# Performance work log

Measured on AMD Instinct MI355X. Metric: run time of the kernel, lower is better.

## Reference

```python
import jax, jax.numpy as jnp
import numpy as np

DIM = 768
HEADS = 12
HEAD_DIM = DIM // HEADS
HIDDEN = 4 * DIM
EPS = 1e-5


def layernorm(x, g, b):
    mu = jnp.mean(x, axis=-1, keepdims=True)
    var = jnp.var(x, axis=-1, keepdims=True)
    return (x - mu) * jax.lax.rsqrt(var + EPS) * g + b


def setup_inputs() -> dict:
    key = jax.random.key(0)
    ks = jax.random.split(key, 16)
    s = 0.02
    return {
        "x_pre": jax.random.normal(ks[0], (8, 512, DIM), jnp.float32),
        "x_post": jax.random.normal(ks[1], (8, 512, DIM), jnp.float32),
        "attention_mask": jnp.zeros((8, 1, 1024, 1024), jnp.float32),
        "ln1_g": jnp.ones((DIM,), jnp.float32),
        "ln1_b": jnp.zeros((DIM,), jnp.float32),
        "Wq": jax.random.normal(ks[2], (DIM, DIM), jnp.float32) * s,
        "bq": jnp.zeros((DIM,), jnp.float32),
        "Wk": jax.random.normal(ks[3], (DIM, DIM), jnp.float32) * s,
        "bk": jnp.zeros((DIM,), jnp.float32),
        "Wv": jax.random.normal(ks[4], (DIM, DIM), jnp.float32) * s,
        "bv": jnp.zeros((DIM,), jnp.float32),
        "Wo": jax.random.normal(ks[5], (DIM, DIM), jnp.float32) * s,
        "bo": jnp.zeros((DIM,), jnp.float32),
        "ln2_g": jnp.ones((DIM,), jnp.float32),
        "ln2_b": jnp.zeros((DIM,), jnp.float32),
        "W1": jax.random.normal(ks[6], (DIM, HIDDEN), jnp.float32) * s,
        "b1": jnp.zeros((HIDDEN,), jnp.float32),
        "W2": jax.random.normal(ks[7], (HIDDEN, DIM), jnp.float32) * s,
        "b2": jnp.zeros((DIM,), jnp.float32),
        "gamma_1": 0.1 * jnp.ones((DIM,), jnp.float32),
        "gamma_2": 0.1 * jnp.ones((DIM,), jnp.float32),
    }


def reference(x_pre, x_post, attention_mask, ln1_g, ln1_b, Wq, bq, Wk, bk, Wv, bv,
              Wo, bo, ln2_g, ln2_b, W1, b1, W2, b2, gamma_1, gamma_2):
    x = jnp.concatenate((x_pre, x_post), axis=1)  # [B, N, C]
    B, N, C = x.shape
    h = layernorm(x, ln1_g, ln1_b)
    # self-attention with manual QK^T in float32
    q = (h @ Wq + bq).reshape(B, N, HEADS, HEAD_DIM)
    k = (h @ Wk + bk).reshape(B, N, HEADS, HEAD_DIM)
    v = (h @ Wv + bv).reshape(B, N, HEADS, HEAD_DIM)
    scale = HEAD_DIM ** -0.5
    attn = jnp.einsum("bqhd,bkhd->bhqk", q.astype(jnp.float32) * scale,
                      k.astype(jnp.float32)) + attention_mask
    attn = jax.nn.softmax(attn, axis=-1).astype(x.dtype)
    o = jnp.einsum("bhqk,bkhd->bqhd", attn, v).reshape(B, N, C)
    o = o @ Wo + bo
    x = x + gamma_1 * o
    # MLP
    h2 = layernorm(x, ln2_g, ln2_b)
    h2 = jax.nn.gelu(h2 @ W1 + b1, approximate=False) @ W2 + b2
    return x + gamma_2 * h2
```

## Files before the change

### kernel.cpp

```cpp
#include <hip/hip_runtime.h>
#include <hip/hip_fp8.h>
#include <cstdint>
#include <cstddef>

#define BATCH   8
#define SEQ     1024
#define DIMC    768
#define HEADS   12
#define HDIM    64
#define HIDDEN  3072
#define MROWS   (BATCH * SEQ)
#define L2E     1.4426950408889634f

typedef __attribute__((ext_vector_type(8))) short bf16x8;
typedef __attribute__((ext_vector_type(4))) float f32x4;

__device__ __forceinline__ unsigned short f2b(float f) {
    union { float f; unsigned int u; } v; v.f = f;
    unsigned int u = v.u;
    return (unsigned short)((u + 0x7FFFu + ((u >> 16) & 1u)) >> 16);
}
__device__ __forceinline__ unsigned char f2e4m3(float f) {
    __hip_fp8_e4m3 t(f); return t.__x;
}
__device__ __forceinline__ unsigned int b2u(float f) {
    union { float f; unsigned int u; } v; v.f = f; return v.u;
}
__device__ __forceinline__ float u2f(unsigned int u) {
    union { unsigned int u; float f; } v; v.u = u; return v.f;
}
__device__ __forceinline__ void gl_lds16(const void* g, void* l) {
    __builtin_amdgcn_global_load_lds(
        (const __attribute__((address_space(1))) unsigned int*)g,
        (__attribute__((address_space(3))) unsigned int*)l, 16, 0, 0);
}
__device__ __forceinline__ float gelu_fast(float x) {
    float p = x * x;
    float a = fmaf(p, 0.044715f, 1.0f);
    float w = x * a * -2.302118131f;
    float z = exp2f(w);
    return x * __builtin_amdgcn_rcpf(1.0f + z);
}

__global__ __launch_bounds__(256) void tcvt_k(const float* __restrict__ src,
                                              unsigned char* __restrict__ dst,
                                              int K, int N) {
    __shared__ float tile[32][33];
    int k0 = blockIdx.y * 32, n0 = blockIdx.x * 32;
    int tx = threadIdx.x, ty = threadIdx.y;
#pragma unroll
    for (int i = 0; i < 4; i++)
        tile[ty + i * 8][tx] = src[(size_t)(k0 + ty + i * 8) * N + n0 + tx];
    __syncthreads();
#pragma unroll
    for (int i = 0; i < 4; i++)
        dst[(size_t)(n0 + ty + i * 8) * K + k0 + tx] = f2e4m3(tile[tx][ty + i * 8]);
}

__global__ __launch_bounds__(256) void tcvt4_k(const float* __restrict__ s0,
                                               const float* __restrict__ s1,
                                               const float* __restrict__ s2,
                                               const float* __restrict__ s3,
                                               unsigned char* __restrict__ d0,
                                               unsigned char* __restrict__ d1,
                                               unsigned char* __restrict__ d2,
                                               unsigned char* __restrict__ d3) {
    const float* src = (blockIdx.z == 0) ? s0 : (blockIdx.z == 1) ? s1
                     : (blockIdx.z == 2) ? s2 : s3;
    unsigned char* dst = (blockIdx.z == 0) ? d0 : (blockIdx.z == 1) ? d1
                       : (blockIdx.z == 2) ? d2 : d3;
    __shared__ float tile[32][33];
    int k0 = blockIdx.y * 32, n0 = blockIdx.x * 32;
    int tx = threadIdx.x, ty = threadIdx.y;
#pragma unroll
    for (int i = 0; i < 4; i++)
        tile[ty + i * 8][tx] = src[(size_t)(k0 + ty + i * 8) * DIMC + n0 + tx];
    __syncthreads();
#pragma unroll
    for (int i = 0; i < 4; i++)
        dst[(size_t)(n0 + ty + i * 8) * DIMC + k0 + tx] = f2e4m3(tile[tx][ty + i * 8]);
}

__global__ __launch_bounds__(256) void vtr_k(const unsigned short* __restrict__ src,
                                             unsigned char* __restrict__ dst) {
    int bh = blockIdx.x, k0 = blockIdx.y * 64;
    __shared__ unsigned short t[64][68];
    const unsigned short* s = src + ((size_t)bh * SEQ + k0) * HDIM;
    unsigned char* d = dst + (size_t)bh * HDIM * SEQ + k0;
    int tid = threadIdx.x;
#pragma unroll
    for (int p = 0; p < 4; p++) {
        int c = p * 256 + tid;
        int key = c >> 4, dd = (c & 15) * 4;
        *(uint2*)&t[key][dd] = *(const uint2*)&s[key * HDIM + dd];
    }
    __syncthreads();
#pragma unroll
    for (int p = 0; p < 8; p++) {
        int idx = p * 256 + tid;
        int dd = idx >> 5, kk = (idx & 31) * 2;
        uchar2 o;
        o.x = f2e4m3(u2f((unsigned int)t[kk][dd] << 16));
        o.y = f2e4m3(u2f((unsigned int)t[kk + 1][dd] << 16));
        *(uchar2*)&d[(size_t)dd * SEQ + kk] = o;
    }
}

__global__ __launch_bounds__(256) void ln_k(const float* __restrict__ xa,
                                            const float* __restrict__ xb,
                                            const float* __restrict__ g,
                                            const float* __restrict__ bt,
                                            float* __restrict__ x_out,
                                            unsigned char* __restrict__ h_out) {
    int r = blockIdx.x;
    const float* src;
    if (xb) {
        int b = r >> 10, nn = r & 1023;
        src = (nn < 512) ? xa + ((size_t)b * 512 + nn) * DIMC
                         : xb + ((size_t)b * 512 + (nn - 512)) * DIMC;
    } else {
        src = xa + (size_t)r * DIMC;
    }
    int t = threadIdx.x;
    float v[3], s = 0.f, s2 = 0.f;
#pragma unroll
    for (int j = 0; j < 3; j++) {
        v[j] = src[t + j * 256];
        s += v[j]; s2 += v[j] * v[j];
    }
#pragma unroll
    for (int off = 32; off > 0; off >>= 1) {
        s  += __shfl_down(s,  off);
        s2 += __shfl_down(s2, off);
    }
    __shared__ float red[8];
    int wid = t >> 6, lane = t & 63;
    if (lane == 0) { red[wid] = s; red[4 + wid] = s2; }
    __syncthreads();
    s  = red[0] + red[1] + red[2] + red[3];
    s2 = red[4] + red[5] + red[6] + red[7];
    float mu  = s * (1.f / DIMC);
    float var = s2 * (1.f / DIMC) - mu * mu;
    float rstd = rsqrtf(var + 1e-5f);
#pragma unroll
    for (int j = 0; j < 3; j++) {
        int i = t + j * 256;
        float xv = v[j];
        if (x_out) x_out[(size_t)r * DIMC + i] = xv;
        h_out[(size_t)r * DIMC + i] = f2e4m3((xv - mu) * rstd * g[i] + bt[i]);
    }
}

template <int MODE, int TM>
__global__ __launch_bounds__(256) void gemm_k(
    const unsigned char* __restrict__ A,
    const unsigned char* __restrict__ Bt0,
    const unsigned char* __restrict__ Bt1,
    const unsigned char* __restrict__ Bt2,
    const float* __restrict__ bias0,
    const float* __restrict__ bias1,
    const float* __restrict__ bias2,
    const float* __restrict__ resid,
    const float* __restrict__ gamma,
    float* __restrict__ outf,
    unsigned short* __restrict__ outb0,
    unsigned short* __restrict__ outb1,
    unsigned short* __restrict__ outb2,
    unsigned char* __restrict__ outc,
    int K, int ldo) {

    constexpr int AI = TM / 32;
    const int tid  = threadIdx.x;
    const int wid  = tid >> 6, lane = tid & 63;
    const int quad = lane >> 4, l16 = lane & 15;
    const int m0 = blockIdx.y * TM, n0 = blockIdx.x * 128;
    const int waveM = (wid >> 1) * (AI * 16), waveN = (wid & 1) * 64;

    const unsigned char* Bt = Bt0;
    if (MODE == 0) Bt = (blockIdx.z == 0) ? Bt0 : (blockIdx.z == 1) ? Bt1 : Bt2;

    __shared__ __align__(16) unsigned char As[TM * 128];
    __shared__ __align__(16) unsigned char Bs[128 * 128];

    int carow[AI], caoff[AI], cbrow[4], cboff[4];
#pragma unroll
    for (int j = 0; j < AI; j++) {
        int c = j * 256 + tid;
        carow[j] = c >> 3;
        caoff[j] = ((c & 7) ^ (carow[j] & 7)) * 16;
    }
#pragma unroll
    for (int j = 0; j < 4; j++) {
        int c = j * 256 + tid;
        cbrow[j] = c >> 3;
        cboff[j] = ((c & 7) ^ (cbrow[j] & 7)) * 16;
    }
    const int asw = l16 & 7;
    int abase[AI], bbase[4];
#pragma unroll
    for (int i = 0; i < AI; i++)
        abase[i] = (waveM + i * 16 + l16) * 128 + (quad & 1) * 8;
#pragma unroll
    for (int i = 0; i < 4; i++)
        bbase[i] = (waveN + i * 16 + l16) * 128 + (quad & 1) * 8;

    f32x4 acc[AI][4] = {};

    for (int k0 = 0; k0 < K; k0 += 128) {
#pragma unroll
        for (int j = 0; j < AI; j++)
            gl_lds16(&A[(size_t)(m0 + carow[j]) * K + k0 + caoff[j]],
                     &As[(j * 256 + wid * 64) * 16]);
#pragma unroll
        for (int j = 0; j < 4; j++)
            gl_lds16(&Bt[(size_t)(n0 + cbrow[j]) * K + k0 + cboff[j]],
                     &Bs[(j * 256 + wid * 64) * 16]);
        __syncthreads();

#pragma unroll
        for (int kk = 0; kk < 4; kk++) {
            const int csw = ((kk * 2 + (quad >> 1)) ^ asw) * 16;
            long a[AI], b[4];
#pragma unroll
            for (int i = 0; i < AI; i++) a[i] = *(const long*)&As[abase[i] + csw];
#pragma unroll
            for (int i = 0; i < 4; i++) b[i] = *(const long*)&Bs[bbase[i] + csw];
#pragma unroll
            for (int i = 0; i < AI; i++)
#pragma unroll
                for (int j = 0; j < 4; j++)
                    acc[i][j] = __builtin_amdgcn_mfma_f32_16x16x32_fp8_fp8(
                        a[i], b[j], acc[i][j], 0, 0, 0);
        }
        __syncthreads();
    }

    const float* bias = bias0;
    unsigned short* outb = outb0;
    if (MODE == 0) {
        bias = (blockIdx.z == 0) ? bias0 : (blockIdx.z == 1) ? bias1 : bias2;
        outb = (blockIdx.z == 0) ? outb0 : (blockIdx.z == 1) ? outb1 : outb2;
    }
    const float qscale = 0.125f * L2E;
#pragma unroll
    for (int i = 0; i < AI; i++) {
#pragma unroll
        for (int j = 0; j < 4; j++) {
            int n = n0 + waveN + j * 16 + l16;
#pragma unroll
            for (int r = 0; r < 4; r++) {
                int m = m0 + waveM + i * 16 + quad * 4 + r;
                float val = acc[i][j][r];
                if (MODE == 0) {
                    val += bias[n];
                    if (blockIdx.z == 0) val *= qscale;
                    int bb = m >> 10, nn = m & 1023;
                    int hh = n >> 6,  d  = n & 63;
                    outb[(((size_t)bb * HEADS + hh) * SEQ + nn) * HDIM + d] = f2b(val);
                } else if (MODE == 1 || MODE == 3) {
                    val += bias[n];
                    outf[(size_t)m * ldo + n] =
                        resid[(size_t)m * ldo + n] + gamma[n] * val;
                } else {
                    outc[(size_t)m * ldo + n] = f2e4m3(gelu_fast(val + bias[n]));
                }
            }
        }
    }
}

__global__ __launch_bounds__(256) void attn_k(const unsigned short* __restrict__ Q,
                                              const unsigned short* __restrict__ Km,
                                              const unsigned char* __restrict__ Vt,
                                              const float* __restrict__ mask,
                                              unsigned char* __restrict__ O) {
    const int bh = blockIdx.x;
    const int b = bh / HEADS, h = bh - b * HEADS;
    const int tid = threadIdx.x;
    const int wid = tid >> 6, lane = tid & 63;
    const int quad = lane >> 4, l16 = lane & 15;
    const int qw = blockIdx.y * 64 + wid * 16;

    __shared__ __align__(16) unsigned short Ks[128 * 64];
    __shared__ __align__(16) unsigned char  Vs[64 * 128];
    __shared__ __align__(16) unsigned char  Ps[4][16 * 136];
    unsigned char* sp = Ps[wid];

    const unsigned short* Qp = Q + ((size_t)bh * SEQ + qw) * HDIM;
    bf16x8 aQ[2];
    aQ[0] = *(const bf16x8*)(Qp + l16 * HDIM + quad * 8);
    aQ[1] = *(const bf16x8*)(Qp + l16 * HDIM + 32 + quad * 8);

    int kql[4], vql[2];
#pragma unroll
    for (int j = 0; j < 4; j++) {
        int ck = (wid * 4 + j) * 64 + lane;
        int key = ck >> 3, ch = ck & 7;
        kql[j] = key * HDIM + ((ch ^ ((key >> 3) & 7)) * 8);
    }
#pragma unroll
    for (int j = 0; j < 2; j++) {
        int cv = j * 256 + wid * 64 + lane;
        int d = cv >> 3, ch = cv & 7;
        vql[j] = d * SEQ + ((ch ^ (d & 7)) * 16);
    }
    const unsigned short* Kb = Km + (size_t)bh * SEQ * HDIM;
    const unsigned char*  Vb = Vt + (size_t)bh * HDIM * SEQ;
    const float* Mbase = mask + (size_t)b * SEQ * SEQ
                       + (size_t)(qw + quad * 4) * SEQ + 8 * l16;

    f32x4 o[4] = {};
    f32x4 osum = {};
    const long ONES = 0x3838383838383838L;

    for (int key0 = 0; key0 < SEQ; key0 += 128) {
        float mreg[4][8];
        const float* mb = Mbase + key0;
#pragma unroll
        for (int r = 0; r < 4; r++) {
            float4 u0 = *(const float4*)(mb + r * SEQ);
            float4 u1 = *(const float4*)(mb + r * SEQ + 4);
            mreg[r][0] = u0.x; mreg[r][1] = u0.y; mreg[r][2] = u0.z; mreg[r][3] = u0.w;
            mreg[r][4] = u1.x; mreg[r][5] = u1.y; mreg[r][6] = u1.z; mreg[r][7] = u1.w;
        }
        const unsigned short* Kg = Kb + (size_t)key0 * HDIM;
        const unsigned char*  Vg = Vb + key0;
#pragma unroll
        for (int j = 0; j < 4; j++)
            gl_lds16(Kg + kql[j], &Ks[(wid * 4 + j) * 512]);
#pragma unroll
        for (int j = 0; j < 2; j++)
            gl_lds16(Vg + vql[j], &Vs[(j * 256 + wid * 64) * 16]);
        __syncthreads();

        f32x4 s[8];
#pragma unroll
        for (int nt = 0; nt < 8; nt++) {
            const unsigned short* kp = &Ks[(8 * l16 + nt) * 64];
            bf16x8 b0 = *(const bf16x8*)&kp[(quad ^ (l16 & 7)) * 8];
            bf16x8 b1 = *(const bf16x8*)&kp[((4 + quad) ^ (l16 & 7)) * 8];
            f32x4 t = {};
            t = __builtin_amdgcn_mfma_f32_16x16x32_bf16(aQ[0], b0, t, 0, 0, 0);
            t = __builtin_amdgcn_mfma_f32_16x16x32_bf16(aQ[1], b1, t, 0, 0, 0);
            s[nt] = t;
        }

#pragma unroll
        for (int r = 0; r < 4; r++) {
            float e[8];
#pragma unroll
            for (int nt = 0; nt < 8; nt++)
                e[nt] = exp2f(fmaf(mreg[r][nt], L2E, s[nt][r]));
            unsigned int d0 = __builtin_amdgcn_cvt_pk_fp8_f32(e[0], e[1], 0, false);
            d0 = __builtin_amdgcn_cvt_pk_fp8_f32(e[2], e[3], d0, true);
            unsigned int d1 = __builtin_amdgcn_cvt_pk_fp8_f32(e[4], e[5], 0, false);
            d1 = __builtin_amdgcn_cvt_pk_fp8_f32(e[6], e[7], d1, true);
            int prow = quad * 4 + r;
            uint2 pv; pv.x = d0; pv.y = d1;
            *(uint2*)&sp[prow * 136 + ((l16 ^ (prow & 7)) * 8)] = pv;
        }
        __builtin_amdgcn_wave_barrier();

        long aP[4];
#pragma unroll
        for (int kt = 0; kt < 4; kt++)
            aP[kt] = *(const long*)&sp[l16 * 136 + (((kt * 4 + quad) ^ (l16 & 7)) * 8)];
#pragma unroll
        for (int kt = 0; kt < 4; kt++)
            osum = __builtin_amdgcn_mfma_f32_16x16x32_fp8_fp8(aP[kt], ONES, osum, 0, 0, 0);
#pragma unroll
        for (int dt = 0; dt < 4; dt++) {
            const unsigned char* vp = &Vs[(dt * 16 + l16) * 128];
            f32x4 oo = o[dt];
#pragma unroll
            for (int kt = 0; kt < 4; kt++) {
                long bv = *(const long*)
                    &vp[(((kt * 2 + (quad >> 1)) ^ (l16 & 7)) * 16) + (quad & 1) * 8];
                oo = __builtin_amdgcn_mfma_f32_16x16x32_fp8_fp8(aP[kt], bv, oo, 0, 0, 0);
            }
            o[dt] = oo;
        }
        __syncthreads();
    }

#pragma unroll
    for (int r = 0; r < 4; r++) {
        float inv = 1.0f / osum[r];
#pragma unroll
        for (int dt = 0; dt < 4; dt++)
            O[(size_t)(b * SEQ + qw + quad * 4 + r) * DIMC + h * HDIM + dt * 16 + l16] =
                f2e4m3(o[dt][r] * inv);
    }
}

extern "C" void kernel_launch(void* const* d_in, const int* in_sizes, int n_in,
                              void* d_out, int out_size, void* d_ws, size_t ws_size,
                              hipStream_t stream) {
    const float* x_pre = (const float*)d_in[0];
    const float* x_post= (const float*)d_in[1];
    const float* mask  = (const float*)d_in[2];
    const float* ln1g  = (const float*)d_in[3];
    const float* ln1b  = (const float*)d_in[4];
    const float* Wq    = (const float*)d_in[5];
    const float* bq    = (const float*)d_in[6];
    const float* Wk    = (const float*)d_in[7];
    const float* bk    = (const float*)d_in[8];
    const float* Wv    = (const float*)d_in[9];
    const float* bv    = (const float*)d_in[10];
    const float* Wo    = (const float*)d_in[11];
    const float* bo    = (const float*)d_in[12];
    const float* ln2g  = (const float*)d_in[13];
    const float* ln2b  = (const float*)d_in[14];
    const float* W1    = (const float*)d_in[15];
    const float* b1    = (const float*)d_in[16];
    const float* W2    = (const float*)d_in[17];
    const float* b2    = (const float*)d_in[18];
    const float* g1    = (const float*)d_in[19];
    const float* g2    = (const float*)d_in[20];
    float* out = (float*)d_out;

    char* p = (char*)d_ws;
    float* xf  = (float*)p;                  p += (size_t)MROWS * DIMC * 4;
    float* x2f = (float*)p;                  p += (size_t)MROWS * DIMC * 4;
    unsigned char* h8  = (unsigned char*)p;  p += (size_t)MROWS * DIMC;
    unsigned char* O8  = (unsigned char*)p;  p += (size_t)MROWS * DIMC;
    unsigned char* G8  = (unsigned char*)p;  p += (size_t)MROWS * HIDDEN;
    unsigned short* Qb = (unsigned short*)p; p += (size_t)MROWS * DIMC * 2;
    unsigned short* Kb = (unsigned short*)p; p += (size_t)MROWS * DIMC * 2;
    unsigned short* Vb = (unsigned short*)p; p += (size_t)MROWS * DIMC * 2;
    unsigned char* V8  = (unsigned char*)p;  p += (size_t)MROWS * DIMC;
    unsigned char* Wq8 = (unsigned char*)p;  p += (size_t)DIMC * DIMC;
    unsigned char* Wk8 = (unsigned char*)p;  p += (size_t)DIMC * DIMC;
    unsigned char* Wv8 = (unsigned char*)p;  p += (size_t)DIMC * DIMC;
    unsigned char* Wo8 = (unsigned char*)p;  p += (size_t)DIMC * DIMC;
    unsigned char* W18 = (unsigned char*)p;  p += (size_t)DIMC * HIDDEN;
    unsigned char* W28 = (unsigned char*)p;  p += (size_t)DIMC * HIDDEN;

    dim3 tb(32, 8);
    tcvt4_k<<<dim3(24, 24, 4), tb, 0, stream>>>(Wq, Wk, Wv, Wo, Wq8, Wk8, Wv8, Wo8);
    tcvt_k<<<dim3(96, 24), tb, 0, stream>>>(W1, W18, DIMC, HIDDEN);
    tcvt_k<<<dim3(24, 96), tb, 0, stream>>>(W2, W28, HIDDEN, DIMC);

    ln_k<<<MROWS, 256, 0, stream>>>(x_pre, x_post, ln1g, ln1b, xf, h8);

    gemm_k<0, 128><<<dim3(6, 64, 3), 256, 0, stream>>>(h8, Wq8, Wk8, Wv8,
        bq, bk, bv, nullptr, nullptr, nullptr, Qb, Kb, Vb, nullptr, DIMC, DIMC);

    vtr_k<<<dim3(96, 16), 256, 0, stream>>>(Vb, V8);

    attn_k<<<dim3(96, 16), 256, 0, stream>>>(Qb, Kb, V8, mask, O8);

    gemm_k<1, 64><<<dim3(6, 128), 256, 0, stream>>>(O8, Wo8, nullptr, nullptr,
        bo, nullptr, nullptr, xf, g1, x2f, nullptr, nullptr, nullptr, nullptr, DIMC, DIMC);

    ln_k<<<MROWS, 256, 0, stream>>>(x2f, nullptr, ln2g, ln2b, nullptr, h8);

    gemm_k<2, 128><<<dim3(24, 64), 256, 0, stream>>>(h8, W18, nullptr, nullptr,
        b1, nullptr, nullptr, nullptr, nullptr, nullptr, nullptr, nullptr, nullptr,
        G8, DIMC, HIDDEN);

    gemm_k<3, 64><<<dim3(6, 128), 256, 0, stream>>>(G8, W28, nullptr, nullptr,
        b2, nullptr, nullptr, x2f, g2, out, nullptr, nullptr, nullptr, nullptr,
        HIDDEN, DIMC);

    (void)in_sizes; (void)n_in; (void)out_size; (void)ws_size;
}
```

Before: 381.4 us.

## Double-buffer K/V tiles in attention and remap blocks so each XCD serves one batch

The attention kernel now ping-pongs two LDS buffers for K and V and prefetches the next mask tile into registers while the current tile is computed, so global-to-LDS loads overlap the MFMA and exp work. Block indices are also remapped so that blocks landing on the same XCD (flat index mod 8) all handle one batch, aiming for better L2 reuse of that batch's mask and K/V. In exchange, LDS use doubles and register pressure grows from holding two mask tiles, which may lower occupancy. The remap assumes a grid of 96 by 16 blocks.

```diff
diff --git a/kernel.cpp b/kernel.cpp
--- a/kernel.cpp
+++ b/kernel.cpp
@@ -269,20 +269,80 @@
     }
 }
 
+__device__ __forceinline__ void attn_tile(
+    const unsigned short* __restrict__ KsB,
+    const unsigned char*  __restrict__ VsB,
+    unsigned char* __restrict__ sp,
+    bf16x8 aQ0, bf16x8 aQ1,
+    const float (&M)[4][8],
+    int quad, int l16,
+    f32x4 (&o)[4], f32x4& osum)
+{
+    const long ONES = 0x3838383838383838L;
+    f32x4 s[8];
+#pragma unroll
+    for (int nt = 0; nt < 8; nt++) {
+        const unsigned short* kp = &KsB[(8 * l16 + nt) * 64];
+        bf16x8 b0 = *(const bf16x8*)&kp[(quad ^ (l16 & 7)) * 8];
+        bf16x8 b1 = *(const bf16x8*)&kp[((4 + quad) ^ (l16 & 7)) * 8];
+        f32x4 t = {};
+        t = __builtin_amdgcn_mfma_f32_16x16x32_bf16(aQ0, b0, t, 0, 0, 0);
+        t = __builtin_amdgcn_mfma_f32_16x16x32_bf16(aQ1, b1, t, 0, 0, 0);
+        s[nt] = t;
+    }
+#pragma unroll
+    for (int r = 0; r < 4; r++) {
+        float e[8];
+#pragma unroll
+        for (int nt = 0; nt < 8; nt++)
+            e[nt] = exp2f(fmaf(M[r][nt], L2E, s[nt][r]));
+        unsigned int d0 = __builtin_amdgcn_cvt_pk_fp8_f32(e[0], e[1], 0, false);
+        d0 = __builtin_amdgcn_cvt_pk_fp8_f32(e[2], e[3], d0, true);
+        unsigned int d1 = __builtin_amdgcn_cvt_pk_fp8_f32(e[4], e[5], 0, false);
+        d1 = __builtin_amdgcn_cvt_pk_fp8_f32(e[6], e[7], d1, true);
+        int prow = quad * 4 + r;
+        uint2 pv; pv.x = d0; pv.y = d1;
+        *(uint2*)&sp[prow * 136 + ((l16 ^ (prow & 7)) * 8)] = pv;
+    }
+    __builtin_amdgcn_wave_barrier();
+    long aP[4];
+#pragma unroll
+    for (int kt = 0; kt < 4; kt++)
+        aP[kt] = *(const long*)&sp[l16 * 136 + (((kt * 4 + quad) ^ (l16 & 7)) * 8)];
+#pragma unroll
+    for (int kt = 0; kt < 4; kt++)
+        osum = __builtin_amdgcn_mfma_f32_16x16x32_fp8_fp8(aP[kt], ONES, osum, 0, 0, 0);
+#pragma unroll
+    for (int dt = 0; dt < 4; dt++) {
+        const unsigned char* vp = &VsB[(dt * 16 + l16) * 128];
+        f32x4 oo = o[dt];
+#pragma unroll
+        for (int kt = 0; kt < 4; kt++) {
+            long bv = *(const long*)
+                &vp[(((kt * 2 + (quad >> 1)) ^ (l16 & 7)) * 16) + (quad & 1) * 8];
+            oo = __builtin_amdgcn_mfma_f32_16x16x32_fp8_fp8(aP[kt], bv, oo, 0, 0, 0);
+        }
+        o[dt] = oo;
+    }
+}
+
 __global__ __launch_bounds__(256) void attn_k(const unsigned short* __restrict__ Q,
                                               const unsigned short* __restrict__ Km,
                                               const unsigned char* __restrict__ Vt,
                                               const float* __restrict__ mask,
                                               unsigned char* __restrict__ O) {
-    const int bh = blockIdx.x;
-    const int b = bh / HEADS, h = bh - b * HEADS;
+    const int flat = blockIdx.y * 96 + blockIdx.x;
+    const int xcd  = flat & 7, slot = flat >> 3;
+    const int h = slot % 12, y = slot / 12;
+    const int b = xcd;
+    const int bh = b * HEADS + h;
     const int tid = threadIdx.x;
     const int wid = tid >> 6, lane = tid & 63;
     const int quad = lane >> 4, l16 = lane & 15;
-    const int qw = blockIdx.y * 64 + wid * 16;
-
-    __shared__ __align__(16) unsigned short Ks[128 * 64];
-    __shared__ __align__(16) unsigned char  Vs[64 * 128];
+    const int qw = y * 64 + wid * 16;
+
+    __shared__ __align__(16) unsigned short Ks[2][128 * 64];
+    __shared__ __align__(16) unsigned char  Vs[2][64 * 128];
     __shared__ __align__(16) unsigned char  Ps[4][16 * 136];
     unsigned char* sp = Ps[wid];
 
@@ -309,79 +369,52 @@
     const float* Mbase = mask + (size_t)b * SEQ * SEQ
                        + (size_t)(qw + quad * 4) * SEQ + 8 * l16;
 
+#define ATTN_STAGE(BUF, K0) do {                                              \
+        const unsigned short* Kg_ = Kb + (size_t)(K0) * HDIM;                 \
+        const unsigned char*  Vg_ = Vb + (K0);                                \
+        _Pragma("unroll")                                                     \
+        for (int j = 0; j < 4; j++)                                           \
+            gl_lds16(Kg_ + kql[j], &Ks[BUF][(wid * 4 + j) * 512]);            \
+        _Pragma("unroll")                                                     \
+        for (int j = 0; j < 2; j++)                                           \
+            gl_lds16(Vg_ + vql[j], &Vs[BUF][(j * 256 + wid * 64) * 16]);      \
+    } while (0)
+
+#define ATTN_MASK(M, K0) do {                                                 \
+        const float* mb_ = Mbase + (K0);                                      \
+        _Pragma("unroll")                                                     \
+        for (int r = 0; r < 4; r++) {                                         \
+            float4 u0 = *(const float4*)(mb_ + r * SEQ);                      \
+            float4 u1 = *(const float4*)(mb_ + r * SEQ + 4);                  \
+            M[r][0] = u0.x; M[r][1] = u0.y; M[r][2] = u0.z; M[r][3] = u0.w;   \
+            M[r][4] = u1.x; M[r][5] = u1.y; M[r][6] = u1.z; M[r][7] = u1.w;   \
+        }                                                                     \
+    } while (0)
+
     f32x4 o[4] = {};
     f32x4 osum = {};
-    const long ONES = 0x3838383838383838L;
-
-    for (int key0 = 0; key0 < SEQ; key0 += 128) {
-        float mreg[4][8];
-        const float* mb = Mbase + key0;
-#pragma unroll
-        for (int r = 0; r < 4; r++) {
-            float4 u0 = *(const float4*)(mb + r * SEQ);
-            float4 u1 = *(const float4*)(mb + r * SEQ + 4);
-            mreg[r][0] = u0.x; mreg[r][1] = u0.y; mreg[r][2] = u0.z; mreg[r][3] = u0.w;
-            mreg[r][4] = u1.x; mreg[r][5] = u1.y; mreg[r][6] = u1.z; mreg[r][7] = u1.w;
+    float mA[4][8], mB[4][8];
+
+    ATTN_STAGE(0, 0);
+    ATTN_MASK(mA, 0);
+    __syncthreads();
+
+#pragma unroll
+    for (int t2 = 0; t2 < SEQ / 256; t2++) {
+        const int te = t2 * 256;
+        ATTN_STAGE(1, te + 128);
+        ATTN_MASK(mB, te + 128);
+        attn_tile(Ks[0], Vs[0], sp, aQ[0], aQ[1], mA, quad, l16, o, osum);
+        __syncthreads();
+        if (t2 + 1 < SEQ / 256) {
+            ATTN_STAGE(0, te + 256);
+            ATTN_MASK(mA, te + 256);
         }
-        const unsigned short* Kg = Kb + (size_t)key0 * HDIM;
-        const unsigned char*  Vg = Vb + key0;
-#pragma unroll
-        for (int j = 0; j < 4; j++)
-            gl_lds16(Kg + kql[j], &Ks[(wid * 4 + j) * 512]);
-#pragma unroll
-        for (int j = 0; j < 2; j++)
-            gl_lds16(Vg + vql[j], &Vs[(j * 256 + wid * 64) * 16]);
+        attn_tile(Ks[1], Vs[1], sp, aQ[0], aQ[1], mB, quad, l16, o, osum);
         __syncthreads();
-
-        f32x4 s[8];
-#pragma unroll
-        for (int nt = 0; nt < 8; nt++) {
-            const unsigned short* kp = &Ks[(8 * l16 + nt) * 64];
-            bf16x8 b0 = *(const bf16x8*)&kp[(quad ^ (l16 & 7)) * 8];
-            bf16x8 b1 = *(const bf16x8*)&kp[((4 + quad) ^ (l16 & 7)) * 8];
-            f32x4 t = {};
-            t = __builtin_amdgcn_mfma_f32_16x16x32_bf16(aQ[0], b0, t, 0, 0, 0);
-            t = __builtin_amdgcn_mfma_f32_16x16x32_bf16(aQ[1], b1, t, 0, 0, 0);
-            s[nt] = t;
-        }
-
-#pragma unroll
-        for (int r = 0; r < 4; r++) {
-            float e[8];
-#pragma unroll
-            for (int nt = 0; nt < 8; nt++)
-                e[nt] = exp2f(fmaf(mreg[r][nt], L2E, s[nt][r]));
-            unsigned int d0 = __builtin_amdgcn_cvt_pk_fp8_f32(e[0], e[1], 0, false);
-            d0 = __builtin_amdgcn_cvt_pk_fp8_f32(e[2], e[3], d0, true);
-            unsigned int d1 = __builtin_amdgcn_cvt_pk_fp8_f32(e[4], e[5], 0, false);
-            d1 = __builtin_amdgcn_cvt_pk_fp8_f32(e[6], e[7], d1, true);
-            int prow = quad * 4 + r;
-            uint2 pv; pv.x = d0; pv.y = d1;
-            *(uint2*)&sp[prow * 136 + ((l16 ^ (prow & 7)) * 8)] = pv;
-        }
-        __builtin_amdgcn_wave_barrier();
-
-        long aP[4];
-#pragma unroll
-        for (int kt = 0; kt < 4; kt++)
-            aP[kt] = *(const long*)&sp[l16 * 136 + (((kt * 4 + quad) ^ (l16 & 7)) * 8)];
-#pragma unroll
-        for (int kt = 0; kt < 4; kt++)
-            osum = __builtin_amdgcn_mfma_f32_16x16x32_fp8_fp8(aP[kt], ONES, osum, 0, 0, 0);
-#pragma unroll
-        for (int dt = 0; dt < 4; dt++) {
-            const unsigned char* vp = &Vs[(dt * 16 + l16) * 128];
-            f32x4 oo = o[dt];
-#pragma unroll
-            for (int kt = 0; kt < 4; kt++) {
-                long bv = *(const long*)
-                    &vp[(((kt * 2 + (quad >> 1)) ^ (l16 & 7)) * 16) + (quad & 1) * 8];
-                oo = __builtin_amdgcn_mfma_f32_16x16x32_fp8_fp8(aP[kt], bv, oo, 0, 0, 0);
-            }
-            o[dt] = oo;
-        }
-        __syncthreads();
-    }
+    }
+#undef ATTN_STAGE
+#undef ATTN_MASK
 
 #pragma unroll
     for (int r = 0; r < 4; r++) {
```

New measurement: 381.4 us. About the same (-0.0%).

## Prefetch next K/V tile into registers and remap attention blocks per XCD

Applied to the files above, without the earlier changes.

The attention kernel now software-pipelines K/V loading. The next tile is loaded into registers during compute on the current one and written to LDS after a barrier, replacing direct global-to-LDS copies followed by a sync. It also splits the score computation into two halves so exp/convert work interleaves with the MFMAs, and remaps the flat block index so each batch maps to one XCD for L2 locality. Launch bounds request 4 blocks per CU, which raises register pressure risk alongside the extra prefetch registers.

```diff
diff --git a/kernel.cpp b/kernel.cpp
--- a/kernel.cpp
+++ b/kernel.cpp
@@ -269,17 +269,20 @@
     }
 }
 
-__global__ __launch_bounds__(256) void attn_k(const unsigned short* __restrict__ Q,
-                                              const unsigned short* __restrict__ Km,
-                                              const unsigned char* __restrict__ Vt,
-                                              const float* __restrict__ mask,
-                                              unsigned char* __restrict__ O) {
-    const int bh = blockIdx.x;
-    const int b = bh / HEADS, h = bh - b * HEADS;
+__global__ __launch_bounds__(256, 4) void attn_k(const unsigned short* __restrict__ Q,
+                                                 const unsigned short* __restrict__ Km,
+                                                 const unsigned char* __restrict__ Vt,
+                                                 const float* __restrict__ mask,
+                                                 unsigned char* __restrict__ O) {
+    const int flat = blockIdx.y * 96 + blockIdx.x;
+    const int xcd  = flat & 7, slot = flat >> 3;
+    const int h = slot % 12, y = slot / 12;
+    const int b = xcd;
+    const int bh = b * HEADS + h;
     const int tid = threadIdx.x;
     const int wid = tid >> 6, lane = tid & 63;
     const int quad = lane >> 4, l16 = lane & 15;
-    const int qw = blockIdx.y * 64 + wid * 16;
+    const int qw = y * 64 + wid * 16;
 
     __shared__ __align__(16) unsigned short Ks[128 * 64];
     __shared__ __align__(16) unsigned char  Vs[64 * 128];
@@ -291,72 +294,107 @@
     aQ[0] = *(const bf16x8*)(Qp + l16 * HDIM + quad * 8);
     aQ[1] = *(const bf16x8*)(Qp + l16 * HDIM + 32 + quad * 8);
 
-    int kql[4], vql[2];
+    int kqb[4], vqb[2];
 #pragma unroll
     for (int j = 0; j < 4; j++) {
         int ck = (wid * 4 + j) * 64 + lane;
         int key = ck >> 3, ch = ck & 7;
-        kql[j] = key * HDIM + ((ch ^ ((key >> 3) & 7)) * 8);
+        kqb[j] = key * 128 + ((ch ^ ((key >> 3) & 7)) * 16);
     }
 #pragma unroll
     for (int j = 0; j < 2; j++) {
         int cv = j * 256 + wid * 64 + lane;
         int d = cv >> 3, ch = cv & 7;
-        vql[j] = d * SEQ + ((ch ^ (d & 7)) * 16);
-    }
-    const unsigned short* Kb = Km + (size_t)bh * SEQ * HDIM;
-    const unsigned char*  Vb = Vt + (size_t)bh * HDIM * SEQ;
+        vqb[j] = d * SEQ + ((ch ^ (d & 7)) * 16);
+    }
+    const char* Kb = (const char*)(Km + (size_t)bh * SEQ * HDIM);
+    const char* Vb = (const char*)(Vt + (size_t)bh * HDIM * SEQ);
     const float* Mbase = mask + (size_t)b * SEQ * SEQ
                        + (size_t)(qw + quad * 4) * SEQ + 8 * l16;
+
+    uint4 kst[4], vst[2];
+#define ATTN_LOADR(K0) do {                                                   \
+        const char* Kg_ = Kb + (size_t)(K0) * 128;                            \
+        const char* Vg_ = Vb + (K0);                                          \
+        _Pragma("unroll")                                                     \
+        for (int j = 0; j < 4; j++)                                           \
+            kst[j] = *(const uint4*)(Kg_ + kqb[j]);                           \
+        _Pragma("unroll")                                                     \
+        for (int j = 0; j < 2; j++)                                           \
+            vst[j] = *(const uint4*)(Vg_ + vqb[j]);                           \
+    } while (0)
+
+#define ATTN_WRITER() do {                                                    \
+        _Pragma("unroll")                                                     \
+        for (int j = 0; j < 4; j++)                                           \
+            *(uint4*)((char*)Ks + (wid * 4 + j) * 1024 + lane * 16) = kst[j]; \
+        _Pragma("unroll")                                                     \
+        for (int j = 0; j < 2; j++)                                           \
+            *(uint4*)((char*)Vs + (j * 256 + wid * 64 + lane) * 16) = vst[j]; \
+    } while (0)
 
     f32x4 o[4] = {};
     f32x4 osum = {};
     const long ONES = 0x3838383838383838L;
 
-    for (int key0 = 0; key0 < SEQ; key0 += 128) {
-        float mreg[4][8];
-        const float* mb = Mbase + key0;
+    ATTN_LOADR(0);
+    ATTN_WRITER();
+    __syncthreads();
+
+#pragma unroll
+    for (int t = 0; t < SEQ / 128; t++) {
+        if (t < SEQ / 128 - 1) ATTN_LOADR((t + 1) * 128);
+
+        const float* mb_ = Mbase + t * 128;
+        float4 mu0[4], mu1[4];
 #pragma unroll
         for (int r = 0; r < 4; r++) {
-            float4 u0 = *(const float4*)(mb + r * SEQ);
-            float4 u1 = *(const float4*)(mb + r * SEQ + 4);
-            mreg[r][0] = u0.x; mreg[r][1] = u0.y; mreg[r][2] = u0.z; mreg[r][3] = u0.w;
-            mreg[r][4] = u1.x; mreg[r][5] = u1.y; mreg[r][6] = u1.z; mreg[r][7] = u1.w;
-        }
-        const unsigned short* Kg = Kb + (size_t)key0 * HDIM;
-        const unsigned char*  Vg = Vb + key0;
-#pragma unroll
-        for (int j = 0; j < 4; j++)
-            gl_lds16(Kg + kql[j], &Ks[(wid * 4 + j) * 512]);
-#pragma unroll
-        for (int j = 0; j < 2; j++)
-            gl_lds16(Vg + vql[j], &Vs[(j * 256 + wid * 64) * 16]);
-        __syncthreads();
-
-        f32x4 s[8];
-#pragma unroll
-        for (int nt = 0; nt < 8; nt++) {
+            mu0[r] = *(const float4*)(mb_ + r * SEQ);
+            mu1[r] = *(const float4*)(mb_ + r * SEQ + 4);
+        }
+
+        f32x4 sA[4];
+#pragma unroll
+        for (int nt = 0; nt < 4; nt++) {
             const unsigned short* kp = &Ks[(8 * l16 + nt) * 64];
             bf16x8 b0 = *(const bf16x8*)&kp[(quad ^ (l16 & 7)) * 8];
             bf16x8 b1 = *(const bf16x8*)&kp[((4 + quad) ^ (l16 & 7)) * 8];
-            f32x4 t = {};
-            t = __builtin_amdgcn_mfma_f32_16x16x32_bf16(aQ[0], b0, t, 0, 0, 0);
-            t = __builtin_amdgcn_mfma_f32_16x16x32_bf16(aQ[1], b1, t, 0, 0, 0);
-            s[nt] = t;
-        }
-
+            f32x4 tt = {};
+            tt = __builtin_amdgcn_mfma_f32_16x16x32_bf16(aQ[0], b0, tt, 0, 0, 0);
+            tt = __builtin_amdgcn_mfma_f32_16x16x32_bf16(aQ[1], b1, tt, 0, 0, 0);
+            sA[nt] = tt;
+        }
+        unsigned int dlo[4];
 #pragma unroll
         for (int r = 0; r < 4; r++) {
-            float e[8];
-#pragma unroll
-            for (int nt = 0; nt < 8; nt++)
-                e[nt] = exp2f(fmaf(mreg[r][nt], L2E, s[nt][r]));
-            unsigned int d0 = __builtin_amdgcn_cvt_pk_fp8_f32(e[0], e[1], 0, false);
-            d0 = __builtin_amdgcn_cvt_pk_fp8_f32(e[2], e[3], d0, true);
-            unsigned int d1 = __builtin_amdgcn_cvt_pk_fp8_f32(e[4], e[5], 0, false);
-            d1 = __builtin_amdgcn_cvt_pk_fp8_f32(e[6], e[7], d1, true);
+            float e0 = exp2f(fmaf(mu0[r].x, L2E, sA[0][r]));
+            float e1 = exp2f(fmaf(mu0[r].y, L2E, sA[1][r]));
+            float e2 = exp2f(fmaf(mu0[r].z, L2E, sA[2][r]));
+            float e3 = exp2f(fmaf(mu0[r].w, L2E, sA[3][r]));
+            unsigned int d0 = __builtin_amdgcn_cvt_pk_fp8_f32(e0, e1, 0, false);
+            dlo[r] = __builtin_amdgcn_cvt_pk_fp8_f32(e2, e3, d0, true);
+        }
+        f32x4 sB[4];
+#pragma unroll
+        for (int nt = 0; nt < 4; nt++) {
+            const unsigned short* kp = &Ks[(8 * l16 + 4 + nt) * 64];
+            bf16x8 b0 = *(const bf16x8*)&kp[(quad ^ (l16 & 7)) * 8];
+            bf16x8 b1 = *(const bf16x8*)&kp[((4 + quad) ^ (l16 & 7)) * 8];
+            f32x4 tt = {};
+            tt = __builtin_amdgcn_mfma_f32_16x16x32_bf16(aQ[0], b0, tt, 0, 0, 0);
+            tt = __builtin_amdgcn_mfma_f32_16x16x32_bf16(aQ[1], b1, tt, 0, 0, 0);
+            sB[nt] = tt;
+        }
+#pragma unroll
+        for (int r = 0; r < 4; r++) {
+            float e4 = exp2f(fmaf(mu1[r].x, L2E, sB[0][r]));
+            float e5 = exp2f(fmaf(mu1[r].y, L2E, sB[1][r]));
+            float e6 = exp2f(fmaf(mu1[r].z, L2E, sB[2][r]));
+            float e7 = exp2f(fmaf(mu1[r].w, L2E, sB[3][r]));
+            unsigned int d1 = __builtin_amdgcn_cvt_pk_fp8_f32(e4, e5, 0, false);
+            d1 = __builtin_amdgcn_cvt_pk_fp8_f32(e6, e7, d1, true);
             int prow = quad * 4 + r;
-            uint2 pv; pv.x = d0; pv.y = d1;
+            uint2 pv; pv.x = dlo[r]; pv.y = d1;
             *(uint2*)&sp[prow * 136 + ((l16 ^ (prow & 7)) * 8)] = pv;
         }
         __builtin_amdgcn_wave_barrier();
@@ -380,8 +418,15 @@
             }
             o[dt] = oo;
         }
+
         __syncthreads();
-    }
+        if (t < SEQ / 128 - 1) {
+            ATTN_WRITER();
+            __syncthreads();
+        }
+    }
+#undef ATTN_LOADR
+#undef ATTN_WRITER
 
 #pragma unroll
     for (int r = 0; r < 4; r++) {
```

After: 449.6 us. 17.9% more time.

## Double-buffer attention K/V tiles in LDS and remap blocks across XCDs

Applied to the files above, without the earlier changes.

The attention kernel now processes 64-key tiles with two LDS buffers, prefetching the next K/V tile while computing the current one, instead of a single 128-key buffer loaded and synchronised each iteration. Block indices are also remapped so blocks of the same batch land on the same XCD, aiming at better L2 reuse of K/V and the mask. Swizzle patterns and P-tile layout are adjusted to the smaller tile. It trades more loop iterations and barriers for overlapped loads, and it depends on the grid being launched as 96 by y.

```diff
diff --git a/kernel.cpp b/kernel.cpp
--- a/kernel.cpp
+++ b/kernel.cpp
@@ -274,16 +274,19 @@
                                               const unsigned char* __restrict__ Vt,
                                               const float* __restrict__ mask,
                                               unsigned char* __restrict__ O) {
-    const int bh = blockIdx.x;
-    const int b = bh / HEADS, h = bh - b * HEADS;
+    const int flat = blockIdx.y * 96 + blockIdx.x;
+    const int xcd  = flat & 7, slot = flat >> 3;
+    const int h = slot % 12, y = slot / 12;
+    const int b = xcd;
+    const int bh = b * HEADS + h;
     const int tid = threadIdx.x;
     const int wid = tid >> 6, lane = tid & 63;
     const int quad = lane >> 4, l16 = lane & 15;
-    const int qw = blockIdx.y * 64 + wid * 16;
-
-    __shared__ __align__(16) unsigned short Ks[128 * 64];
-    __shared__ __align__(16) unsigned char  Vs[64 * 128];
-    __shared__ __align__(16) unsigned char  Ps[4][16 * 136];
+    const int qw = y * 64 + wid * 16;
+
+    __shared__ __align__(16) unsigned short Ks[2][64 * 64];
+    __shared__ __align__(16) unsigned char  Vs[2][64 * 64];
+    __shared__ __align__(16) unsigned char  Ps[4][16 * 72];
     unsigned char* sp = Ps[wid];
 
     const unsigned short* Qp = Q + ((size_t)bh * SEQ + qw) * HDIM;
@@ -291,97 +294,99 @@
     aQ[0] = *(const bf16x8*)(Qp + l16 * HDIM + quad * 8);
     aQ[1] = *(const bf16x8*)(Qp + l16 * HDIM + 32 + quad * 8);
 
-    int kql[4], vql[2];
-#pragma unroll
-    for (int j = 0; j < 4; j++) {
-        int ck = (wid * 4 + j) * 64 + lane;
-        int key = ck >> 3, ch = ck & 7;
-        kql[j] = key * HDIM + ((ch ^ ((key >> 3) & 7)) * 8);
-    }
-#pragma unroll
-    for (int j = 0; j < 2; j++) {
-        int cv = j * 256 + wid * 64 + lane;
-        int d = cv >> 3, ch = cv & 7;
-        vql[j] = d * SEQ + ((ch ^ (d & 7)) * 16);
-    }
-    const unsigned short* Kb = Km + (size_t)bh * SEQ * HDIM;
-    const unsigned char*  Vb = Vt + (size_t)bh * HDIM * SEQ;
+    int kqb[2], vqb;
+    {
+#pragma unroll
+        for (int j = 0; j < 2; j++) {
+            int ck = j * 256 + tid;
+            int key = ck >> 3, ch = ck & 7;
+            kqb[j] = key * 128 + ((ch ^ ((key >> 2) & 7)) * 16);
+        }
+        int cv = tid;
+        int d = cv >> 2, c = cv & 3;
+        vqb = d * SEQ + ((c ^ ((d >> 1) & 3)) * 16);
+    }
+    const char* Kb = (const char*)(Km + (size_t)bh * SEQ * HDIM);
+    const char* Vb = (const char*)(Vt + (size_t)bh * HDIM * SEQ);
     const float* Mbase = mask + (size_t)b * SEQ * SEQ
-                       + (size_t)(qw + quad * 4) * SEQ + 8 * l16;
+                       + (size_t)(qw + quad * 4) * SEQ + 4 * l16;
+
+#define ATTN_STAGE(BUF, K0) do {                                              \
+        const char* Kg_ = Kb + (size_t)(K0) * 128;                            \
+        const char* Vg_ = Vb + (K0);                                          \
+        _Pragma("unroll")                                                     \
+        for (int j = 0; j < 2; j++)                                           \
+            gl_lds16(Kg_ + kqb[j], &Ks[BUF][(j * 256 + wid * 64) * 8]);       \
+        gl_lds16(Vg_ + vqb, &Vs[BUF][wid * 1024]);                            \
+    } while (0)
 
     f32x4 o[4] = {};
     f32x4 osum = {};
     const long ONES = 0x3838383838383838L;
-
-    for (int key0 = 0; key0 < SEQ; key0 += 128) {
-        float mreg[4][8];
-        const float* mb = Mbase + key0;
+    const int swk = l16 & 7;
+    const int swv = (l16 >> 1) & 3;
+
+    ATTN_STAGE(0, 0);
+    __syncthreads();
+
+    for (int t = 0; t < SEQ / 64; t++) {
+        const int buf = t & 1;
+        if (t < SEQ / 64 - 1) ATTN_STAGE(buf ^ 1, (t + 1) * 64);
+
+        const float* mb_ = Mbase + t * 64;
+        float4 mreg[4];
+#pragma unroll
+        for (int r = 0; r < 4; r++)
+            mreg[r] = *(const float4*)(mb_ + r * SEQ);
+
+        f32x4 s[4];
+#pragma unroll
+        for (int nt = 0; nt < 4; nt++) {
+            const unsigned short* kp = &Ks[buf][(4 * l16 + nt) * 64];
+            bf16x8 b0 = *(const bf16x8*)&kp[(quad ^ swk) * 8];
+            bf16x8 b1 = *(const bf16x8*)&kp[((4 + quad) ^ swk) * 8];
+            f32x4 tt = {};
+            tt = __builtin_amdgcn_mfma_f32_16x16x32_bf16(aQ[0], b0, tt, 0, 0, 0);
+            tt = __builtin_amdgcn_mfma_f32_16x16x32_bf16(aQ[1], b1, tt, 0, 0, 0);
+            s[nt] = tt;
+        }
+
 #pragma unroll
         for (int r = 0; r < 4; r++) {
-            float4 u0 = *(const float4*)(mb + r * SEQ);
-            float4 u1 = *(const float4*)(mb + r * SEQ + 4);
-            mreg[r][0] = u0.x; mreg[r][1] = u0.y; mreg[r][2] = u0.z; mreg[r][3] = u0.w;
-            mreg[r][4] = u1.x; mreg[r][5] = u1.y; mreg[r][6] = u1.z; mreg[r][7] = u1.w;
-        }
-        const unsigned short* Kg = Kb + (size_t)key0 * HDIM;
-        const unsigned char*  Vg = Vb + key0;
-#pragma unroll
-        for (int j = 0; j < 4; j++)
-            gl_lds16(Kg + kql[j], &Ks[(wid * 4 + j) * 512]);
-#pragma unroll
-        for (int j = 0; j < 2; j++)
-            gl_lds16(Vg + vql[j], &Vs[(j * 256 + wid * 64) * 16]);
-        __syncthreads();
-
-        f32x4 s[8];
-#pragma unroll
-        for (int nt = 0; nt < 8; nt++) {
-            const unsigned short* kp = &Ks[(8 * l16 + nt) * 64];
-            bf16x8 b0 = *(const bf16x8*)&kp[(quad ^ (l16 & 7)) * 8];
-            bf16x8 b1 = *(const bf16x8*)&kp[((4 + quad) ^ (l16 & 7)) * 8];
-            f32x4 t = {};
-            t = __builtin_amdgcn_mfma_f32_16x16x32_bf16(aQ[0], b0, t, 0, 0, 0);
-            t = __builtin_amdgcn_mfma_f32_16x16x32_bf16(aQ[1], b1, t, 0, 0, 0);
-            s[nt] = t;
-        }
-
-#pragma unroll
-        for (int r = 0; r < 4; r++) {
-            float e[8];
-#pragma unroll
-            for (int nt = 0; nt < 8; nt++)
-                e[nt] = exp2f(fmaf(mreg[r][nt], L2E, s[nt][r]));
-            unsigned int d0 = __builtin_amdgcn_cvt_pk_fp8_f32(e[0], e[1], 0, false);
-            d0 = __builtin_amdgcn_cvt_pk_fp8_f32(e[2], e[3], d0, true);
-            unsigned int d1 = __builtin_amdgcn_cvt_pk_fp8_f32(e[4], e[5], 0, false);
-            d1 = __builtin_amdgcn_cvt_pk_fp8_f32(e[6], e[7], d1, true);
+            float e0 = exp2f(fmaf(mreg[r].x, L2E, s[0][r]));
+            float e1 = exp2f(fmaf(mreg[r].y, L2E, s[1][r]));
+            float e2 = exp2f(fmaf(mreg[r].z, L2E, s[2][r]));
+            float e3 = exp2f(fmaf(mreg[r].w, L2E, s[3][r]));
+            unsigned int d0 = __builtin_amdgcn_cvt_pk_fp8_f32(e0, e1, 0, false);
+            d0 = __builtin_amdgcn_cvt_pk_fp8_f32(e2, e3, d0, true);
             int prow = quad * 4 + r;
-            uint2 pv; pv.x = d0; pv.y = d1;
-            *(uint2*)&sp[prow * 136 + ((l16 ^ (prow & 7)) * 8)] = pv;
+            *(unsigned int*)&sp[prow * 72
+                + (((l16 >> 1) ^ (prow & 7)) * 8) + (l16 & 1) * 4] = d0;
         }
         __builtin_amdgcn_wave_barrier();
 
-        long aP[4];
-#pragma unroll
-        for (int kt = 0; kt < 4; kt++)
-            aP[kt] = *(const long*)&sp[l16 * 136 + (((kt * 4 + quad) ^ (l16 & 7)) * 8)];
-#pragma unroll
-        for (int kt = 0; kt < 4; kt++)
+        long aP[2];
+#pragma unroll
+        for (int kt = 0; kt < 2; kt++)
+            aP[kt] = *(const long*)&sp[l16 * 72 + (((kt * 4 + quad) ^ swk) * 8)];
+#pragma unroll
+        for (int kt = 0; kt < 2; kt++)
             osum = __builtin_amdgcn_mfma_f32_16x16x32_fp8_fp8(aP[kt], ONES, osum, 0, 0, 0);
 #pragma unroll
         for (int dt = 0; dt < 4; dt++) {
-            const unsigned char* vp = &Vs[(dt * 16 + l16) * 128];
+            const unsigned char* vp = &Vs[buf][(dt * 16 + l16) * 64];
             f32x4 oo = o[dt];
 #pragma unroll
-            for (int kt = 0; kt < 4; kt++) {
+            for (int kt = 0; kt < 2; kt++) {
                 long bv = *(const long*)
-                    &vp[(((kt * 2 + (quad >> 1)) ^ (l16 & 7)) * 16) + (quad & 1) * 8];
+                    &vp[(((kt * 2 + (quad >> 1)) ^ swv) * 16) + (quad & 1) * 8];
                 oo = __builtin_amdgcn_mfma_f32_16x16x32_fp8_fp8(aP[kt], bv, oo, 0, 0, 0);
             }
             o[dt] = oo;
         }
         __syncthreads();
     }
+#undef ATTN_STAGE
 
 #pragma unroll
     for (int r = 0; r < 4; r++) {
```

Measured after the change: 387.1 us. About the same (+1.5%).
